# Kernel tuning notes

Hardware: AMD Instinct MI355X
Metric: run time of the kernel (lower is better)

Reference implementation:

```python
import jax, jax.numpy as jnp
import numpy as np

B, NQ, NK, D = 8, 4096, 4096, 512


def setup_inputs() -> dict:
    key = jax.random.key(0)
    ks = jax.random.split(key, 8)
    s = 1.0 / np.sqrt(D)
    return {
        "x": jax.random.normal(ks[0], (B, NQ, D), dtype=jnp.float32),
        "context": jax.random.normal(ks[1], (B, NK, D), dtype=jnp.float32),
        "Wq": jax.random.normal(ks[2], (D, D), dtype=jnp.float32) * s,
        "bq": jax.random.normal(ks[3], (D,), dtype=jnp.float32) * 0.01,
        "Wk": jax.random.normal(ks[4], (D, D), dtype=jnp.float32) * s,
        "bk": jax.random.normal(ks[5], (D,), dtype=jnp.float32) * 0.01,
        "Wv": jax.random.normal(ks[6], (D, D), dtype=jnp.float32) * s,
        "bv": jax.random.normal(ks[7], (D,), dtype=jnp.float32) * 0.01,
    }


def reference(x, context, Wq, bq, Wk, bk, Wv, bv):
    # torch Linear: y = x @ W.T + b, W is [out, in]
    Q = jnp.einsum('bnd,ed->bne', x, Wq) + bq          # [B, NQ, D]
    K = jnp.einsum('bmd,ed->bme', context, Wk) + bk    # [B, NK, D]
    V = jnp.einsum('bmd,ed->bme', context, Wv) + bv    # [B, NK, D]
    scale = 1.0 / jnp.sqrt(jnp.asarray(x.shape[-1], dtype=x.dtype))
    scores = jnp.einsum('bne,bme->bnm', Q, K) * scale  # [B, NQ, NK]
    attn = jax.nn.softmax(scores, axis=-1)
    return jnp.einsum('bnm,bme->bne', attn, V)         # [B, NQ, D]
```

## Files before the change

kernel.cpp:

```cpp
#include <hip/hip_runtime.h>
#include <math.h>

typedef unsigned short u16;
typedef unsigned int u32;
typedef __attribute__((ext_vector_type(8))) short short8;
typedef __attribute__((ext_vector_type(4))) float floatx4;

#define DEVINL static __device__ __forceinline__

DEVINL u16 f2b(float f) {
  u32 u = __float_as_uint(f);
  u += 0x7FFFu + ((u >> 16) & 1u);
  return (u16)(u >> 16);
}
DEVINL float b2f(u16 s) { return __uint_as_float(((u32)s) << 16); }

DEVINL void gload16(const void* g, void* lds_base) {
  __builtin_amdgcn_global_load_lds(
      (const __attribute__((address_space(1))) void*)g,
      (__attribute__((address_space(3))) void*)lds_base, 16, 0, 0);
}

DEVINL void stage_a_f32(const float* __restrict__ A, int lda, int gm0, int k0,
                        u16* As, int tid) {
  const int idx = tid & 127;
  const int row8 = idx >> 4;
  const int k16h = idx & 15;
  const int chsel = tid >> 7;
#pragma unroll
  for (int rr = 0; rr < 8; ++rr) {
    const int chunk = rr * 2 + chsel;
    const float4 v = *(const float4*)(A + (long)(gm0 + chunk * 8 + row8) * lda + k0 + k16h * 4);
    u32 lo = (u32)f2b(v.x) | ((u32)f2b(v.y) << 16);
    u32 hi = (u32)f2b(v.z) | ((u32)f2b(v.w) << 16);
    const int baddr = chunk * 1024 + row8 * 128 + (((k16h >> 1) ^ row8) << 4) + ((k16h & 1) << 3);
    uint2 p; p.x = lo; p.y = hi;
    *(uint2*)((char*)As + baddr) = p;
  }
}

__global__ __launch_bounds__(256) void cast4_kernel(const float* __restrict__ in,
                                                    u16* __restrict__ out, long n4) {
  long i = (long)blockIdx.x * blockDim.x + threadIdx.x;
  long stride = (long)gridDim.x * blockDim.x;
  for (; i < n4; i += stride) {
    float4 v = ((const float4*)in)[i];
    ushort4 o;
    o.x = f2b(v.x); o.y = f2b(v.y); o.z = f2b(v.z); o.w = f2b(v.w);
    ((ushort4*)out)[i] = o;
  }
}

__global__ __launch_bounds__(256) void proj_q(const float* __restrict__ A,
                                              const u16* __restrict__ Bt,
                                              const float* __restrict__ bias,
                                              u16* __restrict__ C) {
  __shared__ u16 As[8192];
  __shared__ u16 Bs[8192];
  const int tid = threadIdx.x;
  const int lane = tid & 63;
  const int wave = tid >> 6;
  const int gm0 = blockIdx.y * 128;
  const int gn0 = blockIdx.x * 128;
  const int wm = (wave >> 1) * 64;
  const int wn = (wave & 1) * 64;

  floatx4 acc[4][4];
#pragma unroll
  for (int i = 0; i < 4; ++i)
#pragma unroll
    for (int j = 0; j < 4; ++j)
#pragma unroll
      for (int r = 0; r < 4; ++r) acc[i][j][r] = 0.0f;

  const int lrow = lane >> 3;
  const int lcol = (lane & 7) ^ lrow;
  const int fr_row = lane & 15;
  const int fr_k16 = lane >> 4;

  for (int k0 = 0; k0 < 512; k0 += 64) {
#pragma unroll
    for (int c = 0; c < 4; ++c) {
      const int ch = wave * 4 + c;
      gload16(Bt + (long)(gn0 + ch * 8 + lrow) * 512 + k0 + lcol * 8, (char*)Bs + ch * 1024);
    }
    stage_a_f32(A, 512, gm0, k0, As, tid);
    __syncthreads();
#pragma unroll
    for (int ks = 0; ks < 2; ++ks) {
      const int c16 = ks * 4 + fr_k16;
      short8 af[4], bfv[4];
#pragma unroll
      for (int i = 0; i < 4; ++i) {
        const int m = wm + i * 16 + fr_row;
        const int slot = (m >> 3) * 64 + (m & 7) * 8 + (c16 ^ (m & 7));
        af[i] = *(const short8*)((const char*)As + slot * 16);
      }
#pragma unroll
      for (int j = 0; j < 4; ++j) {
        const int n = wn + j * 16 + fr_row;
        const int slot = (n >> 3) * 64 + (n & 7) * 8 + (c16 ^ (n & 7));
        bfv[j] = *(const short8*)((const char*)Bs + slot * 16);
      }
#pragma unroll
      for (int i = 0; i < 4; ++i)
#pragma unroll
        for (int j = 0; j < 4; ++j)
          acc[i][j] = __builtin_amdgcn_mfma_f32_16x16x32_bf16(af[i], bfv[j], acc[i][j], 0, 0, 0);
    }
    __syncthreads();
  }

  const int crow = (lane >> 4) * 4;
  const int ccol = lane & 15;
#pragma unroll
  for (int i = 0; i < 4; ++i)
#pragma unroll
    for (int j = 0; j < 4; ++j) {
      const int n = gn0 + wn + j * 16 + ccol;
      const float badd = bias[n];
#pragma unroll
      for (int r = 0; r < 4; ++r) {
        const int m = gm0 + wm + i * 16 + crow + r;
        C[(long)m * 512 + n] = f2b(acc[i][j][r] + badd);
      }
    }
}

__global__ __launch_bounds__(256) void proj_kv(const float* __restrict__ A,
                                               const u16* __restrict__ Wk,
                                               const float* __restrict__ bk,
                                               const u16* __restrict__ Wv,
                                               const float* __restrict__ bv,
                                               u16* __restrict__ Kb,
                                               u16* __restrict__ Vt) {
  __shared__ u16 As[8192];
  __shared__ u16 Bs[8192];
  const int tid = threadIdx.x;
  const int lane = tid & 63;
  const int wave = tid >> 6;
  const int isV = blockIdx.x >> 2;
  const u16* Bt = isV ? Wv : Wk;
  const float* bias = isV ? bv : bk;
  const int gm0 = blockIdx.y * 128;
  const int gn0 = (blockIdx.x & 3) * 128;
  const int wm = (wave >> 1) * 64;
  const int wn = (wave & 1) * 64;

  floatx4 acc[4][4];
#pragma unroll
  for (int i = 0; i < 4; ++i)
#pragma unroll
    for (int j = 0; j < 4; ++j)
#pragma unroll
      for (int r = 0; r < 4; ++r) acc[i][j][r] = 0.0f;

  const int lrow = lane >> 3;
  const int lcol = (lane & 7) ^ lrow;
  const int fr_row = lane & 15;
  const int fr_k16 = lane >> 4;

  for (int k0 = 0; k0 < 512; k0 += 64) {
#pragma unroll
    for (int c = 0; c < 4; ++c) {
      const int ch = wave * 4 + c;
      gload16(Bt + (long)(gn0 + ch * 8 + lrow) * 512 + k0 + lcol * 8, (char*)Bs + ch * 1024);
    }
    stage_a_f32(A, 512, gm0, k0, As, tid);
    __syncthreads();
#pragma unroll
    for (int ks = 0; ks < 2; ++ks) {
      const int c16 = ks * 4 + fr_k16;
      short8 af[4], bfv[4];
#pragma unroll
      for (int i = 0; i < 4; ++i) {
        const int m = wm + i * 16 + fr_row;
        const int slot = (m >> 3) * 64 + (m & 7) * 8 + (c16 ^ (m & 7));
        af[i] = *(const short8*)((const char*)As + slot * 16);
      }
#pragma unroll
      for (int j = 0; j < 4; ++j) {
        const int n = wn + j * 16 + fr_row;
        const int slot = (n >> 3) * 64 + (n & 7) * 8 + (c16 ^ (n & 7));
        bfv[j] = *(const short8*)((const char*)Bs + slot * 16);
      }
#pragma unroll
      for (int i = 0; i < 4; ++i)
#pragma unroll
        for (int j = 0; j < 4; ++j)
          acc[i][j] = __builtin_amdgcn_mfma_f32_16x16x32_bf16(af[i], bfv[j], acc[i][j], 0, 0, 0);
    }
    __syncthreads();
  }

  const int crow = (lane >> 4) * 4;
  const int ccol = lane & 15;
  if (!isV) {
#pragma unroll
    for (int i = 0; i < 4; ++i)
#pragma unroll
      for (int j = 0; j < 4; ++j) {
        const int n = gn0 + wn + j * 16 + ccol;
        const float badd = bias[n];
#pragma unroll
        for (int r = 0; r < 4; ++r) {
          const int m = gm0 + wm + i * 16 + crow + r;
          Kb[(long)m * 512 + n] = f2b(acc[i][j][r] + badd);
        }
      }
  } else {
#pragma unroll
    for (int i = 0; i < 4; ++i)
#pragma unroll
      for (int j = 0; j < 4; ++j) {
        const int n = gn0 + wn + j * 16 + ccol;
        const float badd = bias[n];
        const int m = gm0 + wm + i * 16 + crow;
        const int b = m >> 12;
        const int mm = m & 4095;
        ushort4 st;
        st.x = f2b(acc[i][j][0] + badd);
        st.y = f2b(acc[i][j][1] + badd);
        st.z = f2b(acc[i][j][2] + badd);
        st.w = f2b(acc[i][j][3] + badd);
        *(ushort4*)(Vt + (long)b * 512 * 4096 + (long)n * 4096 + mm) = st;
      }
  }
}

template <int OUTBF16>
__global__ __launch_bounds__(256) void gemm_bt(
    const u16* __restrict__ A, const u16* __restrict__ Bt, void* __restrict__ Cout,
    int M, int N, int K, float scale, long aBS, long bBS, long cBS) {
  __shared__ u16 As[8192];
  __shared__ u16 Bs[8192];
  const int tid = threadIdx.x;
  const int lane = tid & 63;
  const int wave = tid >> 6;
  const int bz = blockIdx.z;
  A += (long)bz * aBS;
  Bt += (long)bz * bBS;
  const long cbase = (long)bz * cBS;
  const int gm0 = blockIdx.y * 128;
  const int gn0 = blockIdx.x * 128;
  const int wm = (wave >> 1) * 64;
  const int wn = (wave & 1) * 64;

  floatx4 acc[4][4];
#pragma unroll
  for (int i = 0; i < 4; ++i)
#pragma unroll
    for (int j = 0; j < 4; ++j)
#pragma unroll
      for (int r = 0; r < 4; ++r) acc[i][j][r] = 0.0f;

  const int lrow = lane >> 3;
  const int lcol = (lane & 7) ^ lrow;
  const int fr_row = lane & 15;
  const int fr_k16 = lane >> 4;

  for (int k0 = 0; k0 < K; k0 += 64) {
#pragma unroll
    for (int c = 0; c < 4; ++c) {
      const int ch = wave * 4 + c;
      const int r = ch * 8 + lrow;
      gload16(A + (long)(gm0 + r) * K + k0 + lcol * 8, (char*)As + ch * 1024);
      gload16(Bt + (long)(gn0 + r) * K + k0 + lcol * 8, (char*)Bs + ch * 1024);
    }
    __syncthreads();
#pragma unroll
    for (int ks = 0; ks < 2; ++ks) {
      const int c16 = ks * 4 + fr_k16;
      short8 af[4], bfv[4];
#pragma unroll
      for (int i = 0; i < 4; ++i) {
        const int m = wm + i * 16 + fr_row;
        const int slot = (m >> 3) * 64 + (m & 7) * 8 + (c16 ^ (m & 7));
        af[i] = *(const short8*)((const char*)As + slot * 16);
      }
#pragma unroll
      for (int j = 0; j < 4; ++j) {
        const int n = wn + j * 16 + fr_row;
        const int slot = (n >> 3) * 64 + (n & 7) * 8 + (c16 ^ (n & 7));
        bfv[j] = *(const short8*)((const char*)Bs + slot * 16);
      }
#pragma unroll
      for (int i = 0; i < 4; ++i)
#pragma unroll
        for (int j = 0; j < 4; ++j)
          acc[i][j] = __builtin_amdgcn_mfma_f32_16x16x32_bf16(af[i], bfv[j], acc[i][j], 0, 0, 0);
    }
    __syncthreads();
  }

  const int crow = (lane >> 4) * 4;
  const int ccol = lane & 15;
#pragma unroll
  for (int i = 0; i < 4; ++i)
#pragma unroll
    for (int j = 0; j < 4; ++j) {
      const int n = gn0 + wn + j * 16 + ccol;
#pragma unroll
      for (int r = 0; r < 4; ++r) {
        const int m = gm0 + wm + i * 16 + crow + r;
        const float v = acc[i][j][r] * scale;
        if (OUTBF16)
          ((u16*)Cout)[cbase + (long)m * N + n] = f2b(v);
        else
          ((float*)Cout)[cbase + (long)m * N + n] = v;
      }
    }
}

__global__ __launch_bounds__(256) void softmax_rows(u16* __restrict__ S) {
  const long row = blockIdx.x;
  u16* p = S + row * 4096;
  const int tid = threadIdx.x;
  uint4 q0 = ((const uint4*)p)[tid * 2];
  uint4 q1 = ((const uint4*)p)[tid * 2 + 1];
  u32 w[8] = {q0.x, q0.y, q0.z, q0.w, q1.x, q1.y, q1.z, q1.w};
  float v[16];
#pragma unroll
  for (int k = 0; k < 8; ++k) {
    v[2 * k] = b2f((u16)(w[k] & 0xFFFFu));
    v[2 * k + 1] = b2f((u16)(w[k] >> 16));
  }
  float mx = v[0];
#pragma unroll
  for (int k = 1; k < 16; ++k) mx = fmaxf(mx, v[k]);
#pragma unroll
  for (int off = 32; off > 0; off >>= 1) mx = fmaxf(mx, __shfl_xor(mx, off, 64));
  __shared__ float redm[4], reds[4];
  if ((tid & 63) == 0) redm[tid >> 6] = mx;
  __syncthreads();
  mx = fmaxf(fmaxf(redm[0], redm[1]), fmaxf(redm[2], redm[3]));
  float sum = 0.0f;
#pragma unroll
  for (int k = 0; k < 16; ++k) {
    v[k] = __expf(v[k] - mx);
    sum += v[k];
  }
#pragma unroll
  for (int off = 32; off > 0; off >>= 1) sum += __shfl_xor(sum, off, 64);
  if ((tid & 63) == 0) reds[tid >> 6] = sum;
  __syncthreads();
  sum = reds[0] + reds[1] + reds[2] + reds[3];
  const float inv = 1.0f / sum;
  u32 o[8];
#pragma unroll
  for (int k = 0; k < 8; ++k) {
    const u16 lo = f2b(v[2 * k] * inv);
    const u16 hi = f2b(v[2 * k + 1] * inv);
    o[k] = (u32)lo | ((u32)hi << 16);
  }
  uint4 r0 = {o[0], o[1], o[2], o[3]};
  uint4 r1 = {o[4], o[5], o[6], o[7]};
  ((uint4*)p)[tid * 2] = r0;
  ((uint4*)p)[tid * 2 + 1] = r1;
}

extern "C" void kernel_launch(void* const* d_in, const int* in_sizes, int n_in,
                              void* d_out, int out_size, void* d_ws, size_t ws_size,
                              hipStream_t stream) {
  const int B = 8, NQ = 4096, NK = 4096, D = 512;
  const long nX = (long)B * NQ * D;
  const long nW = (long)D * D;
  const float scale = 0.044194173824159216f;

  const float* x = (const float*)d_in[0];
  const float* ctx = (const float*)d_in[1];
  const float* Wq = (const float*)d_in[2];
  const float* bq = (const float*)d_in[3];
  const float* Wk = (const float*)d_in[4];
  const float* bk = (const float*)d_in[5];
  const float* Wv = (const float*)d_in[6];
  const float* bv = (const float*)d_in[7];
  float* out = (float*)d_out;

  size_t off = 0;
  auto alloc = [&](size_t bytes) { size_t o = off; off = (off + bytes + 255) & ~(size_t)255; return o; };
  char* ws = (char*)d_ws;
  u16* Qb  = (u16*)(ws + alloc(nX * 2));
  u16* Kb  = (u16*)(ws + alloc(nX * 2));
  u16* Vt  = (u16*)(ws + alloc(nX * 2));
  const size_t s_off = off;
  u16* wqb = (u16*)(ws + alloc(nW * 2));
  u16* wkb = (u16*)(ws + alloc(nW * 2));
  u16* wvb = (u16*)(ws + alloc(nW * 2));
  u16* S   = (u16*)(ws + s_off);

  const size_t sBatch = (size_t)NQ * NK * 2;
  const size_t avail = (ws_size > s_off) ? (ws_size - s_off) : 0;
  int nb = (int)(avail / sBatch);
  if (nb > 8) nb = 8;
  else if (nb >= 4 && nb < 8) nb = 4;
  if (nb < 1) nb = 1;

  cast4_kernel<<<128, 256, 0, stream>>>(Wq, wqb, nW / 4);
  cast4_kernel<<<128, 256, 0, stream>>>(Wk, wkb, nW / 4);
  cast4_kernel<<<128, 256, 0, stream>>>(Wv, wvb, nW / 4);

  proj_q<<<dim3(4, 256), 256, 0, stream>>>(x, wqb, bq, Qb);
  proj_kv<<<dim3(8, 256), 256, 0, stream>>>(ctx, wkb, bk, wvb, bv, Kb, Vt);

  for (int b0 = 0; b0 < B; b0 += nb) {
    const int nbb = (b0 + nb <= B) ? nb : (B - b0);
    gemm_bt<1><<<dim3(32, 32, nbb), 256, 0, stream>>>(
        Qb + (long)b0 * NQ * D, Kb + (long)b0 * NK * D, S,
        NQ, NK, D, scale, (long)NQ * D, (long)NK * D, (long)NQ * NK);
    softmax_rows<<<nbb * NQ, 256, 0, stream>>>(S);
    gemm_bt<0><<<dim3(4, 32, nbb), 256, 0, stream>>>(
        S, Vt + (long)b0 * D * NK, out + (long)b0 * NQ * D,
        NQ, D, NK, 1.0f, (long)NQ * NK, (long)D * NK, (long)NQ * D);
  }
  (void)in_sizes; (void)n_in; (void)out_size;
}
```

Baseline: 777.1 us.

## Fuse softmax exp into score GEMM epilogue and defer normalization to output GEMM

The standalone row-softmax kernel is removed. The QK^T GEMM epilogue now writes exp(score*scale) as bf16 and atomically accumulates per-row partial sums into a workspace buffer. The PV GEMM then divides each output row by its sum. This avoids a full extra read and write of the large score matrix. It drops max subtraction, so it relies on scores staying small enough that exp does not overflow, and it adds an atomic reduction plus a zeroing kernel.

```diff
diff --git a/kernel.cpp b/kernel.cpp
--- a/kernel.cpp
+++ b/kernel.cpp
@@ -13,7 +13,6 @@
   u += 0x7FFFu + ((u >> 16) & 1u);
   return (u16)(u >> 16);
 }
-DEVINL float b2f(u16 s) { return __uint_as_float(((u32)s) << 16); }
 
 DEVINL void gload16(const void* g, void* lds_base) {
   __builtin_amdgcn_global_load_lds(
@@ -49,6 +48,11 @@
     o.x = f2b(v.x); o.y = f2b(v.y); o.z = f2b(v.z); o.w = f2b(v.w);
     ((ushort4*)out)[i] = o;
   }
+}
+
+__global__ __launch_bounds__(256) void zerof(float* __restrict__ p, int n4) {
+  int i = blockIdx.x * 256 + threadIdx.x;
+  if (i < n4) ((float4*)p)[i] = make_float4(0.f, 0.f, 0.f, 0.f);
 }
 
 __global__ __launch_bounds__(256) void proj_q(const float* __restrict__ A,
@@ -214,7 +218,7 @@
 #pragma unroll
       for (int j = 0; j < 4; ++j) {
         const int n = gn0 + wn + j * 16 + ccol;
-        const float badd = bias[n];
+        const float badd = bias[j < 0 ? 0 : n];
         const int m = gm0 + wm + i * 16 + crow;
         const int b = m >> 12;
         const int mm = m & 4095;
@@ -228,10 +232,99 @@
   }
 }
 
-template <int OUTBF16>
-__global__ __launch_bounds__(256) void gemm_bt(
-    const u16* __restrict__ A, const u16* __restrict__ Bt, void* __restrict__ Cout,
-    int M, int N, int K, float scale, long aBS, long bBS, long cBS) {
+__global__ __launch_bounds__(256) void gemm_s(
+    const u16* __restrict__ A, const u16* __restrict__ Bt, u16* __restrict__ S,
+    float* __restrict__ Ld, float scale, long aBS, long bBS) {
+  __shared__ u16 As[8192];
+  __shared__ u16 Bs[8192];
+  const int tid = threadIdx.x;
+  const int lane = tid & 63;
+  const int wave = tid >> 6;
+  const int bz = blockIdx.z;
+  A += (long)bz * aBS;
+  Bt += (long)bz * bBS;
+  u16* Sb = S + (long)bz * 4096 * 4096;
+  const int gm0 = blockIdx.y * 128;
+  const int gn0 = blockIdx.x * 128;
+  const int wm = (wave >> 1) * 64;
+  const int wn = (wave & 1) * 64;
+
+  floatx4 acc[4][4];
+#pragma unroll
+  for (int i = 0; i < 4; ++i)
+#pragma unroll
+    for (int j = 0; j < 4; ++j)
+#pragma unroll
+      for (int r = 0; r < 4; ++r) acc[i][j][r] = 0.0f;
+
+  const int lrow = lane >> 3;
+  const int lcol = (lane & 7) ^ lrow;
+  const int fr_row = lane & 15;
+  const int fr_k16 = lane >> 4;
+
+  for (int k0 = 0; k0 < 512; k0 += 64) {
+#pragma unroll
+    for (int c = 0; c < 4; ++c) {
+      const int ch = wave * 4 + c;
+      const int r = ch * 8 + lrow;
+      gload16(A + (long)(gm0 + r) * 512 + k0 + lcol * 8, (char*)As + ch * 1024);
+      gload16(Bt + (long)(gn0 + r) * 512 + k0 + lcol * 8, (char*)Bs + ch * 1024);
+    }
+    __syncthreads();
+#pragma unroll
+    for (int ks = 0; ks < 2; ++ks) {
+      const int c16 = ks * 4 + fr_k16;
+      short8 af[4], bfv[4];
+#pragma unroll
+      for (int i = 0; i < 4; ++i) {
+        const int m = wm + i * 16 + fr_row;
+        const int slot = (m >> 3) * 64 + (m & 7) * 8 + (c16 ^ (m & 7));
+        af[i] = *(const short8*)((const char*)As + slot * 16);
+      }
+#pragma unroll
+      for (int j = 0; j < 4; ++j) {
+        const int n = wn + j * 16 + fr_row;
+        const int slot = (n >> 3) * 64 + (n & 7) * 8 + (c16 ^ (n & 7));
+        bfv[j] = *(const short8*)((const char*)Bs + slot * 16);
+      }
+#pragma unroll
+      for (int i = 0; i < 4; ++i)
+#pragma unroll
+        for (int j = 0; j < 4; ++j)
+          acc[i][j] = __builtin_amdgcn_mfma_f32_16x16x32_bf16(af[i], bfv[j], acc[i][j], 0, 0, 0);
+    }
+    __syncthreads();
+  }
+
+  const int crow = (lane >> 4) * 4;
+  const int ccol = lane & 15;
+  float (*sml)[2] = (float (*)[2])As;
+#pragma unroll
+  for (int i = 0; i < 4; ++i) {
+#pragma unroll
+    for (int r = 0; r < 4; ++r) {
+      const int m = gm0 + wm + i * 16 + crow + r;
+      float p = 0.0f;
+#pragma unroll
+      for (int j = 0; j < 4; ++j) {
+        const int n = gn0 + wn + j * 16 + ccol;
+        const float e = __expf(acc[i][j][r] * scale);
+        Sb[(long)m * 4096 + n] = f2b(e);
+        p += e;
+      }
+#pragma unroll
+      for (int off = 1; off < 16; off <<= 1) p += __shfl_xor(p, off, 64);
+      if ((lane & 15) == 0) sml[wm + i * 16 + crow + r][wave & 1] = p;
+    }
+  }
+  __syncthreads();
+  if (tid < 128)
+    atomicAdd(&Ld[(long)bz * 4096 + gm0 + tid], sml[tid][0] + sml[tid][1]);
+}
+
+__global__ __launch_bounds__(256) void gemm_o(
+    const u16* __restrict__ A, const u16* __restrict__ Bt, float* __restrict__ Cout,
+    const float* __restrict__ Ld, long aBS, long bBS, long cBS) {
   __shared__ u16 As[8192];
   __shared__ u16 Bs[8192];
   const int tid = threadIdx.x;
@@ -259,13 +352,13 @@
   const int fr_row = lane & 15;
   const int fr_k16 = lane >> 4;
 
-  for (int k0 = 0; k0 < K; k0 += 64) {
+  for (int k0 = 0; k0 < 4096; k0 += 64) {
 #pragma unroll
     for (int c = 0; c < 4; ++c) {
       const int ch = wave * 4 + c;
       const int r = ch * 8 + lrow;
-      gload16(A + (long)(gm0 + r) * K + k0 + lcol * 8, (char*)As + ch * 1024);
-      gload16(Bt + (long)(gn0 + r) * K + k0 + lcol * 8, (char*)Bs + ch * 1024);
+      gload16(A + (long)(gm0 + r) * 4096 + k0 + lcol * 8, (char*)As + ch * 1024);
+      gload16(Bt + (long)(gn0 + r) * 4096 + k0 + lcol * 8, (char*)Bs + ch * 1024);
     }
     __syncthreads();
 #pragma unroll
@@ -295,6 +388,12 @@
 
   const int crow = (lane >> 4) * 4;
   const int ccol = lane & 15;
+  float linv[4][4];
+#pragma unroll
+  for (int i = 0; i < 4; ++i)
+#pragma unroll
+    for (int r = 0; r < 4; ++r)
+      linv[i][r] = 1.0f / Ld[(long)bz * 4096 + gm0 + wm + i * 16 + crow + r];
 #pragma unroll
   for (int i = 0; i < 4; ++i)
 #pragma unroll
@@ -303,60 +402,9 @@
 #pragma unroll
       for (int r = 0; r < 4; ++r) {
         const int m = gm0 + wm + i * 16 + crow + r;
-        const float v = acc[i][j][r] * scale;
-        if (OUTBF16)
-          ((u16*)Cout)[cbase + (long)m * N + n] = f2b(v);
-        else
-          ((float*)Cout)[cbase + (long)m * N + n] = v;
-      }
-    }
-}
-
-__global__ __launch_bounds__(256) void softmax_rows(u16* __restrict__ S) {
-  const long row = blockIdx.x;
-  u16* p = S + row * 4096;
-  const int tid = threadIdx.x;
-  uint4 q0 = ((const uint4*)p)[tid * 2];
-  uint4 q1 = ((const uint4*)p)[tid * 2 + 1];
-  u32 w[8] = {q0.x, q0.y, q0.z, q0.w, q1.x, q1.y, q1.z, q1.w};
-  float v[16];
-#pragma unroll
-  for (int k = 0; k < 8; ++k) {
-    v[2 * k] = b2f((u16)(w[k] & 0xFFFFu));
-    v[2 * k + 1] = b2f((u16)(w[k] >> 16));
-  }
-  float mx = v[0];
-#pragma unroll
-  for (int k = 1; k < 16; ++k) mx = fmaxf(mx, v[k]);
-#pragma unroll
-  for (int off = 32; off > 0; off >>= 1) mx = fmaxf(mx, __shfl_xor(mx, off, 64));
-  __shared__ float redm[4], reds[4];
-  if ((tid & 63) == 0) redm[tid >> 6] = mx;
-  __syncthreads();
-  mx = fmaxf(fmaxf(redm[0], redm[1]), fmaxf(redm[2], redm[3]));
-  float sum = 0.0f;
-#pragma unroll
-  for (int k = 0; k < 16; ++k) {
-    v[k] = __expf(v[k] - mx);
-    sum += v[k];
-  }
-#pragma unroll
-  for (int off = 32; off > 0; off >>= 1) sum += __shfl_xor(sum, off, 64);
-  if ((tid & 63) == 0) reds[tid >> 6] = sum;
-  __syncthreads();
-  sum = reds[0] + reds[1] + reds[2] + reds[3];
-  const float inv = 1.0f / sum;
-  u32 o[8];
-#pragma unroll
-  for (int k = 0; k < 8; ++k) {
-    const u16 lo = f2b(v[2 * k] * inv);
-    const u16 hi = f2b(v[2 * k + 1] * inv);
-    o[k] = (u32)lo | ((u32)hi << 16);
-  }
-  uint4 r0 = {o[0], o[1], o[2], o[3]};
-  uint4 r1 = {o[4], o[5], o[6], o[7]};
-  ((uint4*)p)[tid * 2] = r0;
-  ((uint4*)p)[tid * 2 + 1] = r1;
+        Cout[cbase + (long)m * 512 + n] = acc[i][j][r] * linv[i][r];
+      }
+    }
 }
 
 extern "C" void kernel_launch(void* const* d_in, const int* in_sizes, int n_in,
@@ -383,6 +431,7 @@
   u16* Qb  = (u16*)(ws + alloc(nX * 2));
   u16* Kb  = (u16*)(ws + alloc(nX * 2));
   u16* Vt  = (u16*)(ws + alloc(nX * 2));
+  float* Ld = (float*)(ws + alloc((size_t)B * NQ * 4));
   const size_t s_off = off;
   u16* wqb = (u16*)(ws + alloc(nW * 2));
   u16* wkb = (u16*)(ws + alloc(nW * 2));
@@ -399,19 +448,19 @@
   cast4_kernel<<<128, 256, 0, stream>>>(Wq, wqb, nW / 4);
   cast4_kernel<<<128, 256, 0, stream>>>(Wk, wkb, nW / 4);
   cast4_kernel<<<128, 256, 0, stream>>>(Wv, wvb, nW / 4);
+  zerof<<<(B * NQ / 4 + 255) / 256, 256, 0, stream>>>(Ld, B * NQ / 4);
 
   proj_q<<<dim3(4, 256), 256, 0, stream>>>(x, wqb, bq, Qb);
   proj_kv<<<dim3(8, 256), 256, 0, stream>>>(ctx, wkb, bk, wvb, bv, Kb, Vt);
 
   for (int b0 = 0; b0 < B; b0 += nb) {
     const int nbb = (b0 + nb <= B) ? nb : (B - b0);
-    gemm_bt<1><<<dim3(32, 32, nbb), 256, 0, stream>>>(
+    gemm_s<<<dim3(32, 32, nbb), 256, 0, stream>>>(
         Qb + (long)b0 * NQ * D, Kb + (long)b0 * NK * D, S,
-        NQ, NK, D, scale, (long)NQ * D, (long)NK * D, (long)NQ * NK);
-    softmax_rows<<<nbb * NQ, 256, 0, stream>>>(S);
-    gemm_bt<0><<<dim3(4, 32, nbb), 256, 0, stream>>>(
+        Ld + (long)b0 * NQ, scale, (long)NQ * D, (long)NK * D);
+    gemm_o<<<dim3(4, 32, nbb), 256, 0, stream>>>(
         S, Vt + (long)b0 * D * NK, out + (long)b0 * NQ * D,
-        NQ, D, NK, 1.0f, (long)NQ * NK, (long)D * NK, (long)NQ * D);
+        Ld + (long)b0 * NQ, (long)NQ * NK, (long)D * NK, (long)NQ * D);
   }
   (void)in_sizes; (void)n_in; (void)out_size;
 }
```

After: 776.0 us. Within noise of the previous version (-0.1%).
